# Performance work log

Measured on AMD Instinct MI355X. Metric: run time of the kernel, lower is better.

Reference implementation:

```python
import jax, jax.numpy as jnp
import numpy as np

GRID = 32          # latent grid points per dim
N_OUT = 16384      # output query points
BATCH = 2
C = 256            # projection_channels (latent hidden width)
D = 3              # gno_coord_dim
OUT_CH = 4         # out_channels
RADIUS = 0.045     # gno_radius


def _radius_neighbors(x, y, r):
    """Radius ball search: for each query x_i find all y_j with ||x_i-y_j||<=r.
    Returns (nb_index, out_index) edge lists, sorted by query (CSR order)."""
    r2 = np.float32(r * r)
    nb_idx, out_idx = [], []
    for s in range(0, x.shape[0], 512):  # chunk to bound memory
        d2 = ((x[s:s + 512, None, :] - y[None, :, :]) ** 2).sum(-1)
        oi, yi = np.nonzero(d2 <= r2)
        out_idx.append((oi + s).astype(np.int32))
        nb_idx.append(yi.astype(np.int32))
    return np.concatenate(nb_idx), np.concatenate(out_idx)


def setup_inputs() -> dict:
    key = jax.random.key(0)
    ks = jax.random.split(key, 8)
    # latent queries: regular grid on [0,1]^3
    g = np.linspace(0.0, 1.0, GRID, dtype=np.float32)
    gx, gy, gz = np.meshgrid(g, g, g, indexing="ij")
    grid = np.stack([gx, gy, gz], axis=-1)               # (G,G,G,3)
    latent_queries = jnp.asarray(grid[None])             # (1,G,G,G,3)
    output_queries = jax.random.uniform(ks[0], (1, N_OUT, D), dtype=jnp.float32)
    nb_idx, out_idx = _radius_neighbors(np.asarray(output_queries[0]),
                                        grid.reshape(-1, D), RADIUS)
    latent_embed = jax.random.normal(ks[1], (BATCH, GRID, GRID, GRID, C), dtype=jnp.float32)

    def lin(k, fi, fo):
        kw, kb = jax.random.split(k)
        W = jax.random.normal(kw, (fi, fo), dtype=jnp.float32) / np.sqrt(fi).astype(np.float32)
        b = jax.random.normal(kb, (fo,), dtype=jnp.float32) * 0.01
        return W, b

    W1, b1 = lin(ks[2], 2 * D, 512)
    W2, b2 = lin(ks[3], 512, 256)
    W3, b3 = lin(ks[4], 256, C)
    Wp, bp = lin(ks[5], C, OUT_CH)
    return {"latent_embed": latent_embed, "latent_queries": latent_queries,
            "output_queries": output_queries,
            "nb_index": jnp.asarray(nb_idx), "out_index": jnp.asarray(out_idx),
            "W1": W1, "b1": b1, "W2": W2, "b2": b2, "W3": W3, "b3": b3,
            "Wp": Wp, "bp": bp}


def reference(latent_embed, latent_queries, output_queries, nb_index, out_index,
              W1, b1, W2, b2, W3, b3, Wp, bp):
    y = latent_queries[0].reshape(-1, latent_queries.shape[-1])   # (n_in, d) grid coords
    x = output_queries[0]                                         # (n_out, d)
    n_out = x.shape[0]
    b = latent_embed.shape[0]
    f_y = latent_embed.reshape(b, -1, latent_embed.shape[-1])     # (b, n_in, c)

    # per-edge kernel MLP on concat(y_j, x_i) -- 'linear' transform type
    agg = jnp.concatenate([y[nb_index], x[out_index]], axis=-1)   # (E, 2d)
    h = jax.nn.gelu(agg @ W1 + b1, approximate=False)             # (E, 512)
    h = jax.nn.gelu(h @ W2 + b2, approximate=False)               # (E, 256)
    k = h @ W3 + b3                                               # (E, c) kernel values

    # k(x_i, y_j) * f(y_j), then mean-reduce over each neighborhood
    msg = k[None, :, :] * f_y[:, nb_index, :]                     # (b, E, c)
    sums = jax.vmap(lambda m: jax.ops.segment_sum(m, out_index, num_segments=n_out))(msg)
    cnt = jax.ops.segment_sum(jnp.ones(nb_index.shape[0], dtype=k.dtype),
                              out_index, num_segments=n_out)
    mean = sums / jnp.maximum(cnt, 1.0)[None, :, None]            # (b, n_out, c)

    # pointwise projection (single Linear, no nonlinearity)
    return mean @ Wp + bp                                         # (b, n_out, out_ch)
```

## Files before the change

kernel.cpp:

```cpp
#include <hip/hip_runtime.h>
#include <math.h>

#define NGRID 32768
#define NOUT  16384
#define CCH   256
#define H1DIM 512
#define TE    64
#define NTHR  512

typedef _Float16 f16x8 __attribute__((ext_vector_type(8)));
typedef float    f32x16 __attribute__((ext_vector_type(16)));

__device__ __forceinline__ unsigned short f32_to_f16_bits(float v) {
    _Float16 h = (_Float16)v;
    return __builtin_bit_cast(unsigned short, h);
}
__device__ __forceinline__ float h2l(unsigned u) {
    return (float)__builtin_bit_cast(_Float16, (unsigned short)(u & 0xffff));
}
__device__ __forceinline__ float h2h(unsigned u) {
    return (float)__builtin_bit_cast(_Float16, (unsigned short)(u >> 16));
}

__device__ __forceinline__ float gelu_fast(float x) {
    float x2 = x * x;
    float u  = x * fmaf(0.035677408f, x2, 0.7978845608f);
    float e  = __builtin_amdgcn_exp2f(u * -2.885390082f);
    return x * __builtin_amdgcn_rcpf(1.0f + e);
}

__global__ __launch_bounds__(256) void gino_pack_kernel(
    const float* __restrict__ W2, const float* __restrict__ W3,
    unsigned short* __restrict__ W2F, unsigned short* __restrict__ W3F)
{
    int idx = blockIdx.x * 256 + threadIdx.x;
    if (idx < 32 * 8 * 64) {
        int l = idx & 63, g = (idx >> 6) & 7, ks = idx >> 9;
        int ch = g * 32 + (l & 31);
        int k0 = ks * 16 + (l >> 5) * 8;
        unsigned int u[4];
        #pragma unroll
        for (int p = 0; p < 4; ++p) {
            unsigned int lo = f32_to_f16_bits(W2[(k0 + 2 * p) * CCH + ch]);
            unsigned int hh = f32_to_f16_bits(W2[(k0 + 2 * p + 1) * CCH + ch]);
            u[p] = lo | (hh << 16);
        }
        *(uint4*)(W2F + idx * 8) = make_uint4(u[0], u[1], u[2], u[3]);
    } else if (idx < 32 * 8 * 64 + 16 * 8 * 64) {
        int i2 = idx - 32 * 8 * 64;
        int l = i2 & 63, g = (i2 >> 6) & 7, ks = i2 >> 9;
        int ch = g * 32 + (l & 31);
        int k0 = ks * 16 + (l >> 5) * 8;
        unsigned int u[4];
        #pragma unroll
        for (int p = 0; p < 4; ++p) {
            unsigned int lo = f32_to_f16_bits(W3[(k0 + 2 * p) * CCH + ch]);
            unsigned int hh = f32_to_f16_bits(W3[(k0 + 2 * p + 1) * CCH + ch]);
            u[p] = lo | (hh << 16);
        }
        *(uint4*)(W3F + i2 * 8) = make_uint4(u[0], u[1], u[2], u[3]);
    }
}

__global__ __launch_bounds__(256) void gino_embed_f16_kernel(
    const float* __restrict__ in, unsigned short* __restrict__ out)
{
    int i = (blockIdx.x * 256 + threadIdx.x) * 8;
    float4 a = *(const float4*)(in + i);
    float4 b = *(const float4*)(in + i + 4);
    unsigned u0 = (unsigned)f32_to_f16_bits(a.x) | ((unsigned)f32_to_f16_bits(a.y) << 16);
    unsigned u1 = (unsigned)f32_to_f16_bits(a.z) | ((unsigned)f32_to_f16_bits(a.w) << 16);
    unsigned u2 = (unsigned)f32_to_f16_bits(b.x) | ((unsigned)f32_to_f16_bits(b.y) << 16);
    unsigned u3 = (unsigned)f32_to_f16_bits(b.z) | ((unsigned)f32_to_f16_bits(b.w) << 16);
    *(uint4*)(out + i) = make_uint4(u0, u1, u2, u3);
}

template <int F16E>
__global__ __launch_bounds__(NTHR, 4) void gino_edge_kernel(
    const float* __restrict__ latent_embed,
    const unsigned short* __restrict__ fembed,
    const float* __restrict__ latent_queries,
    const float* __restrict__ output_queries,
    const int*   __restrict__ nb_index,
    const int*   __restrict__ out_index,
    const float* __restrict__ W1, const float* __restrict__ b1,
    const float* __restrict__ b2, const float* __restrict__ b3,
    const unsigned short* __restrict__ W2F,
    const unsigned short* __restrict__ W3F,
    const float* __restrict__ Wp,
    float* __restrict__ sums, float* __restrict__ cnt, int E)
{
    __shared__ __align__(16) unsigned char s_h1[TE * 256];
    __shared__ __align__(16) unsigned char s_h2[TE * 512];
    __shared__ float s_agg[TE][8];
    __shared__ float s_pm[TE][8];
    __shared__ int s_nb[TE], s_oi[TE], s_valid[TE];

    const int tid = threadIdx.x;
    const int e0  = blockIdx.x * TE;

    ((float*)s_pm)[tid] = 0.0f;
    if (tid < TE) {
        int e     = e0 + tid;
        int valid = (e < E) ? 1 : 0;
        int ec    = valid ? e : (E - 1);
        int nb    = nb_index[ec];
        int oi    = out_index[ec];
        s_nb[tid] = nb; s_oi[tid] = oi; s_valid[tid] = valid;
        s_agg[tid][0] = latent_queries[nb * 3 + 0];
        s_agg[tid][1] = latent_queries[nb * 3 + 1];
        s_agg[tid][2] = latent_queries[nb * 3 + 2];
        s_agg[tid][3] = output_queries[oi * 3 + 0];
        s_agg[tid][4] = output_queries[oi * 3 + 1];
        s_agg[tid][5] = output_queries[oi * 3 + 2];
        if (valid) atomicAdd(&cnt[oi], 1.0f);
    }
    __syncthreads();

    const int l  = tid & 63;
    const int w  = tid >> 6;
    const int le = l & 31;
    const int hi = l >> 5;
    const unsigned bsw1 = (unsigned)(le & 15) << 4;
    const unsigned bsw2 = (unsigned)(le & 31) << 4;

    f32x16 acc0 = {}, acc1 = {};

    #pragma unroll
    for (int c = 0; c < 4; ++c) {
        const unsigned short* gw = W2F + (size_t)(c * 8) * 4096 + w * 512 + l * 8;
        f16x8 a[8];
        #pragma unroll
        for (int ks = 0; ks < 8; ++ks)
            a[ks] = *(const f16x8*)(gw + (size_t)ks * 4096);
        __builtin_amdgcn_sched_barrier(0);

        {
            const int col = c * 128 + l * 2;
            float w0[6], w1v[6];
            #pragma unroll
            for (int i = 0; i < 6; ++i) {
                float2 t2 = *(const float2*)(W1 + i * H1DIM + col);
                w0[i] = t2.x; w1v[i] = t2.y;
            }
            float2 bb = *(const float2*)(b1 + col);
            #pragma unroll
            for (int ee = 0; ee < 8; ++ee) {
                int e = w * 8 + ee;
                float v0 = bb.x, v1 = bb.y;
                #pragma unroll
                for (int i = 0; i < 6; ++i) {
                    float av = s_agg[e][i];
                    v0 = fmaf(av, w0[i], v0);
                    v1 = fmaf(av, w1v[i], v1);
                }
                unsigned u = (unsigned)f32_to_f16_bits(gelu_fast(v0)) |
                             ((unsigned)f32_to_f16_bits(gelu_fast(v1)) << 16);
                *(unsigned*)(s_h1 + e * 256 + (((unsigned)(l * 4)) ^ (((unsigned)(e & 15)) << 4))) = u;
            }
        }
        __syncthreads();

        __builtin_amdgcn_s_setprio(1);
        #pragma unroll
        for (int ks = 0; ks < 8; ++ks) {
            f16x8 b0 = *(const f16x8*)(s_h1 + le * 256 +
                           (((unsigned)(ks * 32 + hi * 16)) ^ bsw1));
            f16x8 b1f = *(const f16x8*)(s_h1 + (32 + le) * 256 +
                           (((unsigned)(ks * 32 + hi * 16)) ^ bsw1));
            acc0 = __builtin_amdgcn_mfma_f32_32x32x16_f16(a[ks], b0,  acc0, 0, 0, 0);
            acc1 = __builtin_amdgcn_mfma_f32_32x32x16_f16(a[ks], b1f, acc1, 0, 0, 0);
        }
        __builtin_amdgcn_s_setprio(0);
        __syncthreads();
    }

    const unsigned short* gw3 = W3F + w * 512 + l * 8;
    f16x8 a3[16];
    #pragma unroll
    for (int ks = 0; ks < 16; ++ks)
        a3[ks] = *(const f16x8*)(gw3 + (size_t)ks * 4096);
    __builtin_amdgcn_sched_barrier(0);

    #pragma unroll
    for (int t = 0; t < 2; ++t) {
        int erow = t * 32 + le;
        unsigned esw = (unsigned)(erow & 31) << 4;
        #pragma unroll
        for (int q = 0; q < 4; ++q) {
            int ch0 = w * 32 + q * 8 + hi * 4;
            float4 bb = *(const float4*)(b2 + ch0);
            float v0 = (t ? acc1[q * 4 + 0] : acc0[q * 4 + 0]) + bb.x;
            float v1 = (t ? acc1[q * 4 + 1] : acc0[q * 4 + 1]) + bb.y;
            float v2 = (t ? acc1[q * 4 + 2] : acc0[q * 4 + 2]) + bb.z;
            float v3 = (t ? acc1[q * 4 + 3] : acc0[q * 4 + 3]) + bb.w;
            unsigned int u0 = f32_to_f16_bits(gelu_fast(v0)) |
                              ((unsigned)f32_to_f16_bits(gelu_fast(v1)) << 16);
            unsigned int u1 = f32_to_f16_bits(gelu_fast(v2)) |
                              ((unsigned)f32_to_f16_bits(gelu_fast(v3)) << 16);
            *(uint2*)(s_h2 + erow * 512 + (((unsigned)(ch0 * 2)) ^ esw)) = make_uint2(u0, u1);
        }
    }
    __syncthreads();

    f32x16 kc0 = {}, kc1 = {};
    __builtin_amdgcn_s_setprio(1);
    #pragma unroll
    for (int ks = 0; ks < 16; ++ks) {
        f16x8 b0 = *(const f16x8*)(s_h2 + le * 512 +
                       (((unsigned)(ks * 32 + hi * 16)) ^ bsw2));
        f16x8 b1f = *(const f16x8*)(s_h2 + (32 + le) * 512 +
                       (((unsigned)(ks * 32 + hi * 16)) ^ bsw2));
        kc0 = __builtin_amdgcn_mfma_f32_32x32x16_f16(a3[ks], b0,  kc0, 0, 0, 0);
        kc1 = __builtin_amdgcn_mfma_f32_32x32x16_f16(a3[ks], b1f, kc1, 0, 0, 0);
    }
    __builtin_amdgcn_s_setprio(0);

    #pragma unroll
    for (int t = 0; t < 2; ++t) {
        int e  = t * 32 + le;
        int nb = s_nb[e];
        float pm[8] = {0.f, 0.f, 0.f, 0.f, 0.f, 0.f, 0.f, 0.f};
        #pragma unroll
        for (int q = 0; q < 4; ++q) {
            int ch0 = w * 32 + q * 8 + hi * 4;
            float4 bb = *(const float4*)(b3 + ch0);
            float kv0 = (t ? kc1[q * 4 + 0] : kc0[q * 4 + 0]) + bb.x;
            float kv1 = (t ? kc1[q * 4 + 1] : kc0[q * 4 + 1]) + bb.y;
            float kv2 = (t ? kc1[q * 4 + 2] : kc0[q * 4 + 2]) + bb.z;
            float kv3 = (t ? kc1[q * 4 + 3] : kc0[q * 4 + 3]) + bb.w;
            float4 f0, f1;
            if constexpr (F16E) {
                const unsigned short* fp = fembed + (size_t)nb * CCH;
                uint2 u0 = *(const uint2*)(fp + ch0);
                uint2 u1 = *(const uint2*)(fp + (size_t)NGRID * CCH + ch0);
                f0 = make_float4(h2l(u0.x), h2h(u0.x), h2l(u0.y), h2h(u0.y));
                f1 = make_float4(h2l(u1.x), h2h(u1.x), h2l(u1.y), h2h(u1.y));
            } else {
                const float* fp = latent_embed + (size_t)nb * CCH;
                f0 = *(const float4*)(fp + ch0);
                f1 = *(const float4*)(fp + (size_t)NGRID * CCH + ch0);
            }
            float4 wp0 = *(const float4*)(Wp + (ch0 + 0) * 4);
            float4 wp1 = *(const float4*)(Wp + (ch0 + 1) * 4);
            float4 wp2 = *(const float4*)(Wp + (ch0 + 2) * 4);
            float4 wp3 = *(const float4*)(Wp + (ch0 + 3) * 4);
            float t0 = kv0 * f0.x, t1 = kv1 * f0.y, t2v = kv2 * f0.z, t3 = kv3 * f0.w;
            pm[0] = fmaf(t0, wp0.x, fmaf(t1, wp1.x, fmaf(t2v, wp2.x, fmaf(t3, wp3.x, pm[0]))));
            pm[1] = fmaf(t0, wp0.y, fmaf(t1, wp1.y, fmaf(t2v, wp2.y, fmaf(t3, wp3.y, pm[1]))));
            pm[2] = fmaf(t0, wp0.z, fmaf(t1, wp1.z, fmaf(t2v, wp2.z, fmaf(t3, wp3.z, pm[2]))));
            pm[3] = fmaf(t0, wp0.w, fmaf(t1, wp1.w, fmaf(t2v, wp2.w, fmaf(t3, wp3.w, pm[3]))));
            float s0 = kv0 * f1.x, s1 = kv1 * f1.y, s2 = kv2 * f1.z, s3 = kv3 * f1.w;
            pm[4] = fmaf(s0, wp0.x, fmaf(s1, wp1.x, fmaf(s2, wp2.x, fmaf(s3, wp3.x, pm[4]))));
            pm[5] = fmaf(s0, wp0.y, fmaf(s1, wp1.y, fmaf(s2, wp2.y, fmaf(s3, wp3.y, pm[5]))));
            pm[6] = fmaf(s0, wp0.z, fmaf(s1, wp1.z, fmaf(s2, wp2.z, fmaf(s3, wp3.z, pm[6]))));
            pm[7] = fmaf(s0, wp0.w, fmaf(s1, wp1.w, fmaf(s2, wp2.w, fmaf(s3, wp3.w, pm[7]))));
        }
        #pragma unroll
        for (int v = 0; v < 8; ++v) pm[v] += __shfl_xor(pm[v], 32);
        if (hi == 0) {
            #pragma unroll
            for (int v = 0; v < 8; ++v) atomicAdd(&s_pm[e][v], pm[v]);
        }
    }
    __syncthreads();

    {
        int el = tid >> 3;
        int v  = tid & 7;
        if (s_valid[el]) {
            int b  = v >> 2;
            int oc = v & 3;
            atomicAdd(&sums[((size_t)b * NOUT + s_oi[el]) * 4 + oc], s_pm[el][v]);
        }
    }
}

__global__ __launch_bounds__(256) void gino_finalize_kernel(
    const float* __restrict__ sums,
    const float* __restrict__ cnt,
    const float* __restrict__ bp,
    float* __restrict__ out)
{
    int idx = blockIdx.x * 256 + threadIdx.x;
    if (idx >= 2 * NOUT * 4) return;
    int oc = idx & 3;
    int i  = (idx >> 2) & (NOUT - 1);
    float c = fmaxf(cnt[i], 1.0f);
    out[idx] = sums[idx] / c + bp[oc];
}

extern "C" void kernel_launch(void* const* d_in, const int* in_sizes, int n_in,
                              void* d_out, int out_size, void* d_ws, size_t ws_size,
                              hipStream_t stream) {
    const float* latent_embed   = (const float*)d_in[0];
    const float* latent_queries = (const float*)d_in[1];
    const float* output_queries = (const float*)d_in[2];
    const int*   nb_index       = (const int*)d_in[3];
    const int*   out_index      = (const int*)d_in[4];
    const float* W1 = (const float*)d_in[5];
    const float* b1 = (const float*)d_in[6];
    const float* W2 = (const float*)d_in[7];
    const float* b2 = (const float*)d_in[8];
    const float* W3 = (const float*)d_in[9];
    const float* b3 = (const float*)d_in[10];
    const float* Wp = (const float*)d_in[11];
    const float* bp = (const float*)d_in[12];

    const int E = in_sizes[3];

    float* sums = (float*)d_ws;
    float* cnt  = sums + 2 * NOUT * 4;
    unsigned short* W2F = (unsigned short*)(cnt + NOUT);
    unsigned short* W3F = W2F + 32 * 8 * 64 * 8;
    unsigned short* fembed = W3F + 16 * 8 * 64 * 8;
    const size_t base_bytes = (size_t)((char*)fembed - (char*)d_ws);
    const size_t femb_bytes = (size_t)2 * NGRID * CCH * 2;
    const bool use_f16 = ws_size >= base_bytes + femb_bytes;

    hipMemsetAsync(d_ws, 0, (size_t)(2 * NOUT * 4 + NOUT) * sizeof(float), stream);

    gino_pack_kernel<<<(32 * 8 * 64 + 16 * 8 * 64 + 255) / 256, 256, 0, stream>>>(
        W2, W3, W2F, W3F);

    int nblk = (E + TE - 1) / TE;
    if (use_f16) {
        gino_embed_f16_kernel<<<(2 * NGRID * CCH / 8 + 255) / 256, 256, 0, stream>>>(
            latent_embed, fembed);
        gino_edge_kernel<1><<<nblk, NTHR, 0, stream>>>(
            latent_embed, fembed, latent_queries, output_queries, nb_index, out_index,
            W1, b1, b2, b3, W2F, W3F, Wp, sums, cnt, E);
    } else {
        gino_edge_kernel<0><<<nblk, NTHR, 0, stream>>>(
            latent_embed, (const unsigned short*)nullptr, latent_queries, output_queries,
            nb_index, out_index, W1, b1, b2, b3, W2F, W3F, Wp, sums, cnt, E);
    }

    gino_finalize_kernel<<<(2 * NOUT * 4 + 255) / 256, 256, 0, stream>>>(
        sums, cnt, bp, (float*)d_out);
}
```

Baseline: 240.1 us.

## Halve edge tile to 32 and split W3 fragment loads to raise occupancy

Shrinks the per-block edge tile from 64 to 32, so each wave keeps one MFMA accumulator per layer instead of two. The W3 weight fragments are now loaded in two halves of eight rather than all sixteen at once, and the launch bounds ask for six blocks per CU instead of four. The aim is lower VGPR and LDS use so more waves can hide latency. The cost is that every block reloads the full W2 and W3 weights for half as many edges, roughly doubling weight traffic and barrier overhead per edge.

```diff
diff --git a/kernel.cpp b/kernel.cpp
--- a/kernel.cpp
+++ b/kernel.cpp
@@ -5,7 +5,7 @@
 #define NOUT  16384
 #define CCH   256
 #define H1DIM 512
-#define TE    64
+#define TE    32
 #define NTHR  512
 
 typedef _Float16 f16x8 __attribute__((ext_vector_type(8)));
@@ -76,7 +76,7 @@
 }
 
 template <int F16E>
-__global__ __launch_bounds__(NTHR, 4) void gino_edge_kernel(
+__global__ __launch_bounds__(NTHR, 6) void gino_edge_kernel(
     const float* __restrict__ latent_embed,
     const unsigned short* __restrict__ fembed,
     const float* __restrict__ latent_queries,
@@ -99,7 +99,7 @@
     const int tid = threadIdx.x;
     const int e0  = blockIdx.x * TE;
 
-    ((float*)s_pm)[tid] = 0.0f;
+    if (tid < TE * 8) ((float*)s_pm)[tid] = 0.0f;
     if (tid < TE) {
         int e     = e0 + tid;
         int valid = (e < E) ? 1 : 0;
@@ -124,7 +124,7 @@
     const unsigned bsw1 = (unsigned)(le & 15) << 4;
     const unsigned bsw2 = (unsigned)(le & 31) << 4;
 
-    f32x16 acc0 = {}, acc1 = {};
+    f32x16 acc = {};
 
     #pragma unroll
     for (int c = 0; c < 4; ++c) {
@@ -145,8 +145,8 @@
             }
             float2 bb = *(const float2*)(b1 + col);
             #pragma unroll
-            for (int ee = 0; ee < 8; ++ee) {
-                int e = w * 8 + ee;
+            for (int ee = 0; ee < 4; ++ee) {
+                int e = w * 4 + ee;
                 float v0 = bb.x, v1 = bb.y;
                 #pragma unroll
                 for (int i = 0; i < 6; ++i) {
@@ -164,71 +164,73 @@
         __builtin_amdgcn_s_setprio(1);
         #pragma unroll
         for (int ks = 0; ks < 8; ++ks) {
-            f16x8 b0 = *(const f16x8*)(s_h1 + le * 256 +
-                           (((unsigned)(ks * 32 + hi * 16)) ^ bsw1));
-            f16x8 b1f = *(const f16x8*)(s_h1 + (32 + le) * 256 +
-                           (((unsigned)(ks * 32 + hi * 16)) ^ bsw1));
-            acc0 = __builtin_amdgcn_mfma_f32_32x32x16_f16(a[ks], b0,  acc0, 0, 0, 0);
-            acc1 = __builtin_amdgcn_mfma_f32_32x32x16_f16(a[ks], b1f, acc1, 0, 0, 0);
+            f16x8 b = *(const f16x8*)(s_h1 + le * 256 +
+                          (((unsigned)(ks * 32 + hi * 16)) ^ bsw1));
+            acc = __builtin_amdgcn_mfma_f32_32x32x16_f16(a[ks], b, acc, 0, 0, 0);
         }
         __builtin_amdgcn_s_setprio(0);
         __syncthreads();
     }
 
     const unsigned short* gw3 = W3F + w * 512 + l * 8;
-    f16x8 a3[16];
-    #pragma unroll
-    for (int ks = 0; ks < 16; ++ks)
-        a3[ks] = *(const f16x8*)(gw3 + (size_t)ks * 4096);
+    f16x8 a3h[8];
+    #pragma unroll
+    for (int ks = 0; ks < 8; ++ks)
+        a3h[ks] = *(const f16x8*)(gw3 + (size_t)ks * 4096);
     __builtin_amdgcn_sched_barrier(0);
 
-    #pragma unroll
-    for (int t = 0; t < 2; ++t) {
-        int erow = t * 32 + le;
-        unsigned esw = (unsigned)(erow & 31) << 4;
+    {
+        unsigned esw = (unsigned)(le & 31) << 4;
         #pragma unroll
         for (int q = 0; q < 4; ++q) {
             int ch0 = w * 32 + q * 8 + hi * 4;
             float4 bb = *(const float4*)(b2 + ch0);
-            float v0 = (t ? acc1[q * 4 + 0] : acc0[q * 4 + 0]) + bb.x;
-            float v1 = (t ? acc1[q * 4 + 1] : acc0[q * 4 + 1]) + bb.y;
-            float v2 = (t ? acc1[q * 4 + 2] : acc0[q * 4 + 2]) + bb.z;
-            float v3 = (t ? acc1[q * 4 + 3] : acc0[q * 4 + 3]) + bb.w;
+            float v0 = acc[q * 4 + 0] + bb.x;
+            float v1 = acc[q * 4 + 1] + bb.y;
+            float v2 = acc[q * 4 + 2] + bb.z;
+            float v3 = acc[q * 4 + 3] + bb.w;
             unsigned int u0 = f32_to_f16_bits(gelu_fast(v0)) |
                               ((unsigned)f32_to_f16_bits(gelu_fast(v1)) << 16);
             unsigned int u1 = f32_to_f16_bits(gelu_fast(v2)) |
                               ((unsigned)f32_to_f16_bits(gelu_fast(v3)) << 16);
-            *(uint2*)(s_h2 + erow * 512 + (((unsigned)(ch0 * 2)) ^ esw)) = make_uint2(u0, u1);
+            *(uint2*)(s_h2 + le * 512 + (((unsigned)(ch0 * 2)) ^ esw)) = make_uint2(u0, u1);
         }
     }
     __syncthreads();
 
-    f32x16 kc0 = {}, kc1 = {};
+    f32x16 kc = {};
     __builtin_amdgcn_s_setprio(1);
     #pragma unroll
-    for (int ks = 0; ks < 16; ++ks) {
-        f16x8 b0 = *(const f16x8*)(s_h2 + le * 512 +
-                       (((unsigned)(ks * 32 + hi * 16)) ^ bsw2));
-        f16x8 b1f = *(const f16x8*)(s_h2 + (32 + le) * 512 +
-                       (((unsigned)(ks * 32 + hi * 16)) ^ bsw2));
-        kc0 = __builtin_amdgcn_mfma_f32_32x32x16_f16(a3[ks], b0,  kc0, 0, 0, 0);
-        kc1 = __builtin_amdgcn_mfma_f32_32x32x16_f16(a3[ks], b1f, kc1, 0, 0, 0);
+    for (int ks = 0; ks < 8; ++ks) {
+        f16x8 b = *(const f16x8*)(s_h2 + le * 512 +
+                      (((unsigned)(ks * 32 + hi * 16)) ^ bsw2));
+        kc = __builtin_amdgcn_mfma_f32_32x32x16_f16(a3h[ks], b, kc, 0, 0, 0);
     }
     __builtin_amdgcn_s_setprio(0);
-
-    #pragma unroll
-    for (int t = 0; t < 2; ++t) {
-        int e  = t * 32 + le;
-        int nb = s_nb[e];
+    #pragma unroll
+    for (int ks = 0; ks < 8; ++ks)
+        a3h[ks] = *(const f16x8*)(gw3 + (size_t)(8 + ks) * 4096);
+    __builtin_amdgcn_sched_barrier(0);
+    __builtin_amdgcn_s_setprio(1);
+    #pragma unroll
+    for (int ks = 0; ks < 8; ++ks) {
+        f16x8 b = *(const f16x8*)(s_h2 + le * 512 +
+                      (((unsigned)((8 + ks) * 32 + hi * 16)) ^ bsw2));
+        kc = __builtin_amdgcn_mfma_f32_32x32x16_f16(a3h[ks], b, kc, 0, 0, 0);
+    }
+    __builtin_amdgcn_s_setprio(0);
+
+    {
+        int nb = s_nb[le];
         float pm[8] = {0.f, 0.f, 0.f, 0.f, 0.f, 0.f, 0.f, 0.f};
         #pragma unroll
         for (int q = 0; q < 4; ++q) {
             int ch0 = w * 32 + q * 8 + hi * 4;
             float4 bb = *(const float4*)(b3 + ch0);
-            float kv0 = (t ? kc1[q * 4 + 0] : kc0[q * 4 + 0]) + bb.x;
-            float kv1 = (t ? kc1[q * 4 + 1] : kc0[q * 4 + 1]) + bb.y;
-            float kv2 = (t ? kc1[q * 4 + 2] : kc0[q * 4 + 2]) + bb.z;
-            float kv3 = (t ? kc1[q * 4 + 3] : kc0[q * 4 + 3]) + bb.w;
+            float kv0 = kc[q * 4 + 0] + bb.x;
+            float kv1 = kc[q * 4 + 1] + bb.y;
+            float kv2 = kc[q * 4 + 2] + bb.z;
+            float kv3 = kc[q * 4 + 3] + bb.w;
             float4 f0, f1;
             if constexpr (F16E) {
                 const unsigned short* fp = fembed + (size_t)nb * CCH;
@@ -260,12 +262,12 @@
         for (int v = 0; v < 8; ++v) pm[v] += __shfl_xor(pm[v], 32);
         if (hi == 0) {
             #pragma unroll
-            for (int v = 0; v < 8; ++v) atomicAdd(&s_pm[e][v], pm[v]);
+            for (int v = 0; v < 8; ++v) atomicAdd(&s_pm[le][v], pm[v]);
         }
     }
     __syncthreads();
 
-    {
+    if (tid < TE * 8) {
         int el = tid >> 3;
         int v  = tid & 7;
         if (s_valid[el]) {
```

After: 513.7 us. +113.9%, slower.
